# Kernel tuning notes

Measured on AMD Instinct MI355X. Metric: run time of the kernel, lower is better.

## Reference

```python
import jax, jax.numpy as jnp
import numpy as np

K = 4  # hard-coded in get_graph_feature


def knn_idx(x, k):
    # x: [B, C, N] -> idx [B, N, k] of nearest neighbors (largest negative sq dist)
    sq = jnp.sum(x * x, axis=1)                      # [B, N]
    inner = jnp.einsum('bcn,bcm->bnm', x, x)          # [B, N, N]
    pd = 2.0 * inner - sq[:, :, None] - sq[:, None, :]  # -||xi-xj||^2
    return jax.lax.top_k(pd, k)[1]                    # [B, N, k]


def get_graph_feature(x, k=K):
    # x: [B, C, N] -> [B, 2C, N, k]
    B = x.shape[0]
    idx = knn_idx(x, k)                               # [B, N, k]
    xt = jnp.transpose(x, (0, 2, 1))                  # [B, N, C]
    nbr = xt[jnp.arange(B)[:, None, None], idx]       # [B, N, k, C]
    ctr = jnp.broadcast_to(xt[:, :, None, :], nbr.shape)
    feat = jnp.concatenate([nbr, ctr], axis=-1)       # [B, N, k, 2C]
    return jnp.transpose(feat, (0, 3, 1, 2))          # [B, 2C, N, k]


def edge_block(x, W):
    # graph feature -> 1x1 conv -> relu -> max over k
    f = get_graph_feature(x)                          # [B, 2C, N, k]
    h = jax.nn.relu(jnp.einsum('oc,bcnk->bonk', W, f))
    return jnp.max(h, axis=-1)                        # [B, O, N]


def setup_inputs() -> dict:
    key = jax.random.key(0)
    ks = jax.random.split(key, 6)
    B, N, emb = 8, 2048, 512
    xavier = lambda k, o, c: jax.random.normal(k, (o, c), jnp.float32) * np.sqrt(2.0 / (o + c))
    return {
        'x': jax.random.normal(ks[0], (B, 3, N), jnp.float32),
        'W1': xavier(ks[1], 64, 6),
        'W2': xavier(ks[2], 64, 128),
        'W3': xavier(ks[3], 128, 128),
        'W4': xavier(ks[4], 256, 256),
        'W5': xavier(ks[5], emb, 512),
    }


def reference(x, W1, W2, W3, W4, W5):
    x1 = edge_block(x, W1)    # [B, 64, N]
    x2 = edge_block(x1, W2)   # [B, 64, N]
    x3 = edge_block(x2, W3)   # [B, 128, N]
    x4 = edge_block(x3, W4)   # [B, 256, N]
    feats = jnp.concatenate([x1, x2, x3, x4], axis=1)  # [B, 512, N]
    # if_relu_atlast=False path: final 1x1 conv, no activation
    return jnp.einsum('oc,bcn->bon', W5, feats)        # [B, emb, N]
```

## Files before the change

### kernel.cpp

```cpp
#include <hip/hip_runtime.h>
#include <hip/hip_bf16.h>

#define B_ 8
#define N_ 2048
#define SEG 8
#define TMM 64
#define TNN 128

typedef __bf16 bf16x8 __attribute__((ext_vector_type(8)));
typedef float  f32x4  __attribute__((ext_vector_type(4)));
typedef unsigned short u16;

__device__ __forceinline__ u16 f2bf(float f) {
    __hip_bfloat16 h = __float2bfloat16(f);
    return *reinterpret_cast<u16*>(&h);
}
__device__ __forceinline__ float bf2f(u16 u) {
    unsigned v = ((unsigned)u) << 16;
    return *reinterpret_cast<float*>(&v);
}

__global__ void k_transpose_x(const float* __restrict__ x, float* __restrict__ xt) {
    int i = blockIdx.x * 256 + threadIdx.x;
    if (i >= B_ * N_) return;
    int b = i >> 11, n = i & (N_ - 1);
    const float* src = x + (size_t)b * 3 * N_ + n;
    float* dst = xt + (size_t)i * 3;
    dst[0] = src[0];
    dst[1] = src[N_];
    dst[2] = src[2 * N_];
}

__global__ void k_sqnorm(const float* __restrict__ act, float* __restrict__ sq, int C) {
    int i = blockIdx.x * 256 + threadIdx.x;
    if (i >= B_ * N_) return;
    const float* r = act + (size_t)i * C;
    float s = 0.f;
    for (int c = 0; c < C; ++c) s += r[c] * r[c];
    sq[i] = s;
}

template<int C, int CP>
__global__ void k_split3(const float* __restrict__ act, u16* __restrict__ xh,
                         u16* __restrict__ xm, u16* __restrict__ xl) {
    int i = blockIdx.x * 256 + threadIdx.x;
    if (i >= B_ * N_ * CP / 8) return;
    int rn = i / (CP / 8), c8 = (i % (CP / 8)) * 8;
    u16 h[8], m[8], l[8];
    #pragma unroll
    for (int j = 0; j < 8; ++j) {
        int c = c8 + j;
        float x = (c < C) ? act[(size_t)rn * C + c] : 0.f;
        u16 hh = f2bf(x);
        float r1 = x - bf2f(hh);
        u16 mm = f2bf(r1);
        float r2 = r1 - bf2f(mm);
        h[j] = hh; m[j] = mm; l[j] = f2bf(r2);
    }
    *(uint4*)&xh[(size_t)i * 8] = *(uint4*)h;
    *(uint4*)&xm[(size_t)i * 8] = *(uint4*)m;
    *(uint4*)&xl[(size_t)i * 8] = *(uint4*)l;
}

__global__ void k_pack_w(const float* __restrict__ W, float* __restrict__ Wt,
                         int O, int C, int ncols, int wrow, int orow0) {
    int i = blockIdx.x * 256 + threadIdx.x;
    if (i >= C * ncols) return;
    int k = i / ncols, o2 = i % ncols;
    int o   = ((o2 < O) ? o2 : o2 - O) + orow0;
    int col = (o2 < O) ? k : (C + k);
    Wt[i] = W[(size_t)o * wrow + col];
}

__device__ __forceinline__ void ins4(float& v0, float& v1, float& v2, float& v3,
                                     int& i0, int& i1, int& i2, int& i3,
                                     float p, int m) {
    bool g3 = p > v3, g2 = p > v2, g1 = p > v1, g0 = p > v0;
    v3 = g2 ? v2 : (g3 ? p : v3); i3 = g2 ? i2 : (g3 ? m : i3);
    v2 = g1 ? v1 : (g2 ? p : v2); i2 = g1 ? i1 : (g2 ? m : i2);
    v1 = g0 ? v0 : (g1 ? p : v1); i1 = g0 ? i0 : (g1 ? m : i1);
    v0 = g0 ? p  : v0;            i0 = g0 ? m  : i0;
}

template<int CP>
__global__ __launch_bounds__(256) void k_knn_mfma(
    const u16* __restrict__ xh, const u16* __restrict__ xmd, const u16* __restrict__ xl,
    const float* __restrict__ sqg, float* __restrict__ pval, int* __restrict__ pidx)
{
    __shared__ __align__(16) u16 sm[3 * TNN * 40 + 3 * TMM * 40];
    __shared__ float sqm_l[TMM];
    u16* Anh = sm;
    u16* Anm = sm + TNN * 40;
    u16* Anl = sm + 2 * TNN * 40;
    u16* Amh = sm + 3 * TNN * 40;
    u16* Amm = Amh + TMM * 40;
    u16* Aml = Amh + 2 * TMM * 40;

    const int bid = blockIdx.x;
    const int seg = bid & (SEG - 1);
    const int nb  = (bid >> 3) & 15;
    const int b   = bid >> 7;
    const int n0  = nb * TNN;
    const int t    = threadIdx.x;
    const int w    = t >> 6, lane = t & 63;
    const int wm = w >> 1, wn = w & 1;
    const int l15 = lane & 15, l4 = lane >> 4;
    const size_t rowbase = (size_t)b * N_;

    float tv[4][4];
    int   ti[4][4];
    #pragma unroll
    for (int ni = 0; ni < 4; ++ni)
        #pragma unroll
        for (int q = 0; q < 4; ++q) { tv[ni][q] = -3.4e38f; ti[ni][q] = 0; }

    const int mstart = seg * (N_ / SEG);
    for (int m0 = mstart; m0 < mstart + N_ / SEG; m0 += TMM) {
        f32x4 acc[2][4];
        #pragma unroll
        for (int mi = 0; mi < 2; ++mi)
            #pragma unroll
            for (int ni = 0; ni < 4; ++ni) acc[mi][ni] = (f32x4){0.f, 0.f, 0.f, 0.f};

        for (int k0 = 0; k0 < CP; k0 += 32) {
            __syncthreads();
            for (int e = t; e < TNN * 4; e += 256) {
                int row = e >> 2, q = e & 3;
                size_t g = (rowbase + n0 + row) * CP + k0 + q * 8;
                int d = row * 40 + q * 8;
                *(uint4*)&Anh[d] = *(const uint4*)&xh[g];
                *(uint4*)&Anm[d] = *(const uint4*)&xmd[g];
                *(uint4*)&Anl[d] = *(const uint4*)&xl[g];
            }
            {
                int row = t >> 2, q = t & 3;
                size_t g = (rowbase + m0 + row) * CP + k0 + q * 8;
                int d = row * 40 + q * 8;
                *(uint4*)&Amh[d] = *(const uint4*)&xh[g];
                *(uint4*)&Amm[d] = *(const uint4*)&xmd[g];
                *(uint4*)&Aml[d] = *(const uint4*)&xl[g];
            }
            if (k0 == 0 && t < TMM) sqm_l[t] = sqg[rowbase + m0 + t];
            __syncthreads();

            bf16x8 amh[2], amm[2], aml[2], bnh[4], bnm[4], bnl[4];
            #pragma unroll
            for (int mi = 0; mi < 2; ++mi) {
                int off = (wm * 32 + mi * 16 + l15) * 40 + l4 * 8;
                amh[mi] = *(const bf16x8*)&Amh[off];
                amm[mi] = *(const bf16x8*)&Amm[off];
                aml[mi] = *(const bf16x8*)&Aml[off];
            }
            #pragma unroll
            for (int ni = 0; ni < 4; ++ni) {
                int off = (wn * 64 + ni * 16 + l15) * 40 + l4 * 8;
                bnh[ni] = *(const bf16x8*)&Anh[off];
                bnm[ni] = *(const bf16x8*)&Anm[off];
                bnl[ni] = *(const bf16x8*)&Anl[off];
            }
            #pragma unroll
            for (int mi = 0; mi < 2; ++mi)
                #pragma unroll
                for (int ni = 0; ni < 4; ++ni) {
                    f32x4 a = acc[mi][ni];
                    a = __builtin_amdgcn_mfma_f32_16x16x32_bf16(amh[mi], bnh[ni], a, 0, 0, 0);
                    a = __builtin_amdgcn_mfma_f32_16x16x32_bf16(amh[mi], bnm[ni], a, 0, 0, 0);
                    a = __builtin_amdgcn_mfma_f32_16x16x32_bf16(amm[mi], bnh[ni], a, 0, 0, 0);
                    a = __builtin_amdgcn_mfma_f32_16x16x32_bf16(amm[mi], bnm[ni], a, 0, 0, 0);
                    a = __builtin_amdgcn_mfma_f32_16x16x32_bf16(amh[mi], bnl[ni], a, 0, 0, 0);
                    a = __builtin_amdgcn_mfma_f32_16x16x32_bf16(aml[mi], bnh[ni], a, 0, 0, 0);
                    acc[mi][ni] = a;
                }
        }
        #pragma unroll
        for (int ni = 0; ni < 4; ++ni)
            #pragma unroll
            for (int mi = 0; mi < 2; ++mi)
                #pragma unroll
                for (int r = 0; r < 4; ++r) {
                    int mloc = wm * 32 + mi * 16 + l4 * 4 + r;
                    float sc = 2.f * acc[mi][ni][r] - sqm_l[mloc];
                    ins4(tv[ni][0], tv[ni][1], tv[ni][2], tv[ni][3],
                         ti[ni][0], ti[ni][1], ti[ni][2], ti[ni][3], sc, m0 + mloc);
                }
    }

    __syncthreads();
    float* sv = (float*)sm;
    int*   si = (int*)sm + 1024;
    #pragma unroll
    for (int ni = 0; ni < 4; ++ni) {
        float v0 = tv[ni][0], v1 = tv[ni][1], v2 = tv[ni][2], v3 = tv[ni][3];
        int   i0 = ti[ni][0], i1 = ti[ni][1], i2 = ti[ni][2], i3 = ti[ni][3];
        #pragma unroll
        for (int st = 16; st < 64; st <<= 1) {
            float w0 = __shfl_xor(v0, st), w1 = __shfl_xor(v1, st);
            float w2 = __shfl_xor(v2, st), w3 = __shfl_xor(v3, st);
            int   j0 = __shfl_xor(i0, st), j1 = __shfl_xor(i1, st);
            int   j2 = __shfl_xor(i2, st), j3 = __shfl_xor(i3, st);
            ins4(v0, v1, v2, v3, i0, i1, i2, i3, w0, j0);
            ins4(v0, v1, v2, v3, i0, i1, i2, i3, w1, j1);
            ins4(v0, v1, v2, v3, i0, i1, i2, i3, w2, j2);
            ins4(v0, v1, v2, v3, i0, i1, i2, i3, w3, j3);
        }
        if (l4 == 0) {
            int col = wn * 64 + ni * 16 + l15;
            int base = (wm * 128 + col) * 4;
            sv[base + 0] = v0; sv[base + 1] = v1; sv[base + 2] = v2; sv[base + 3] = v3;
            si[base + 0] = i0; si[base + 1] = i1; si[base + 2] = i2; si[base + 3] = i3;
        }
    }
    __syncthreads();
    if (t < 128) {
        int b0 = t * 4, b1 = (128 + t) * 4;
        float v0 = sv[b0], v1 = sv[b0 + 1], v2 = sv[b0 + 2], v3 = sv[b0 + 3];
        int   i0 = si[b0], i1 = si[b0 + 1], i2 = si[b0 + 2], i3 = si[b0 + 3];
        #pragma unroll
        for (int q = 0; q < 4; ++q)
            ins4(v0, v1, v2, v3, i0, i1, i2, i3, sv[b1 + q], si[b1 + q]);
        size_t pb = (rowbase + n0 + t) * (SEG * 4) + seg * 4;
        pval[pb + 0] = v0; pval[pb + 1] = v1; pval[pb + 2] = v2; pval[pb + 3] = v3;
        pidx[pb + 0] = i0; pidx[pb + 1] = i1; pidx[pb + 2] = i2; pidx[pb + 3] = i3;
    }
}

__global__ void k_knn_merge(const float* __restrict__ pval, const int* __restrict__ pidx,
                            int* __restrict__ idxo) {
    int rn = blockIdx.x * 256 + threadIdx.x;
    if (rn >= B_ * N_) return;
    const float* pv = pval + (size_t)rn * (SEG * 4);
    const int*   pi = pidx + (size_t)rn * (SEG * 4);
    float v0 = pv[0], v1 = pv[1], v2 = pv[2], v3 = pv[3];
    int   i0 = pi[0], i1 = pi[1], i2 = pi[2], i3 = pi[3];
    for (int s = 1; s < SEG; ++s)
        #pragma unroll
        for (int q = 0; q < 4; ++q)
            ins4(v0, v1, v2, v3, i0, i1, i2, i3, pv[s * 4 + q], pi[s * 4 + q]);
    int* op = idxo + (size_t)rn * 4;
    op[0] = i0; op[1] = i1; op[2] = i2; op[3] = i3;
}

__global__ __launch_bounds__(256) void k_gemm(
    const float* __restrict__ A, int lda,
    const float* __restrict__ Bt, int ldb,
    float* __restrict__ D, int ldd, int K)
{
    __shared__ float At[32 * 68];
    __shared__ float Bs[32 * 68];
    const int r0 = blockIdx.x * 64;
    const int c0 = blockIdx.y * 64;
    const int t  = threadIdx.x;
    const int tr = t >> 4, tc = t & 15;
    float acc[4][4];
    #pragma unroll
    for (int j = 0; j < 4; ++j)
        #pragma unroll
        for (int i = 0; i < 4; ++i) acc[j][i] = 0.f;

    for (int k0 = 0; k0 < K; k0 += 32) {
        for (int e = t; e < 64 * 32; e += 256) {
            int r = e >> 5, kk = e & 31;
            int kg = k0 + kk;
            float v = (kg < K) ? A[(size_t)(r0 + r) * lda + kg] : 0.f;
            At[kk * 68 + r] = v;
        }
        for (int e = t; e < 32 * 16; e += 256) {
            int kk = e >> 4, c4 = (e & 15) << 2;
            int kg = k0 + kk;
            float4 v = {0.f, 0.f, 0.f, 0.f};
            if (kg < K) v = *(const float4*)&Bt[(size_t)kg * ldb + c0 + c4];
            *(float4*)&Bs[kk * 68 + c4] = v;
        }
        __syncthreads();
        for (int kk = 0; kk < 32; ++kk) {
            float4 av = *(float4*)&At[kk * 68 + tr * 4];
            float4 bv = *(float4*)&Bs[kk * 68 + tc * 4];
            const float* ap = (const float*)&av;
            const float* bp = (const float*)&bv;
            #pragma unroll
            for (int j = 0; j < 4; ++j)
                #pragma unroll
                for (int i = 0; i < 4; ++i) acc[j][i] += ap[j] * bp[i];
        }
        __syncthreads();
    }

    #pragma unroll
    for (int j = 0; j < 4; ++j) {
        size_t r = r0 + tr * 4 + j;
        float4 v; v.x = acc[j][0]; v.y = acc[j][1]; v.z = acc[j][2]; v.w = acc[j][3];
        *(float4*)&D[r * ldd + c0 + tc * 4] = v;
    }
}

__global__ void k_gather_max(const float* __restrict__ dot, const int* __restrict__ idxg,
                             float* __restrict__ acto, int O, int ostride, int ocol0) {
    int i = blockIdx.x * 256 + threadIdx.x;
    if (i >= B_ * N_ * O) return;
    int o  = i % O;
    int rn = i / O;
    int b  = rn >> 11;
    const int* ip = idxg + (size_t)rn * 4;
    int twoO = O * 2;
    size_t bbase = (size_t)b * N_ * twoO;
    float ctr = dot[(size_t)rn * twoO + O + o];
    float m0 = dot[bbase + (size_t)ip[0] * twoO + o];
    float m1 = dot[bbase + (size_t)ip[1] * twoO + o];
    float m2 = dot[bbase + (size_t)ip[2] * twoO + o];
    float m3 = dot[bbase + (size_t)ip[3] * twoO + o];
    float mx = fmaxf(fmaxf(m0, m1), fmaxf(m2, m3));
    acto[(size_t)rn * ostride + ocol0 + o] = fmaxf(mx + ctr, 0.f);
}

__global__ void k_feat_bf16(const float* __restrict__ x1, const float* __restrict__ x2,
                            const float* __restrict__ x3, const float* __restrict__ x4,
                            u16* __restrict__ fb) {
    int i = blockIdx.x * 256 + threadIdx.x;
    if (i >= B_ * N_ * 512 / 8) return;
    int rn = i >> 6, c8 = (i & 63) << 3;
    const float* src;
    if      (c8 < 64)  src = x1 + (size_t)rn * 64  + c8;
    else if (c8 < 128) src = x2 + (size_t)rn * 64  + (c8 - 64);
    else if (c8 < 256) src = x3 + (size_t)rn * 128 + (c8 - 128);
    else               src = x4 + (size_t)rn * 256 + (c8 - 256);
    float4 va = *(const float4*)src;
    float4 vb = *(const float4*)(src + 4);
    uint4 u;
    u.x = ((unsigned)f2bf(va.y) << 16) | f2bf(va.x);
    u.y = ((unsigned)f2bf(va.w) << 16) | f2bf(va.z);
    u.z = ((unsigned)f2bf(vb.y) << 16) | f2bf(vb.x);
    u.w = ((unsigned)f2bf(vb.w) << 16) | f2bf(vb.z);
    *(uint4*)&fb[(size_t)i * 8] = u;
}

__global__ void k_w5_bf16(const float* __restrict__ W5, u16* __restrict__ wb) {
    int i = blockIdx.x * 256 + threadIdx.x;
    if (i >= 512 * 512 / 8) return;
    const float* src = W5 + (size_t)i * 8;
    float4 va = *(const float4*)src;
    float4 vb = *(const float4*)(src + 4);
    uint4 u;
    u.x = ((unsigned)f2bf(va.y) << 16) | f2bf(va.x);
    u.y = ((unsigned)f2bf(va.w) << 16) | f2bf(va.z);
    u.z = ((unsigned)f2bf(vb.y) << 16) | f2bf(vb.x);
    u.w = ((unsigned)f2bf(vb.w) << 16) | f2bf(vb.z);
    *(uint4*)&wb[(size_t)i * 8] = u;
}

__global__ __launch_bounds__(256) void k_mfma_final(
    const u16* __restrict__ Ab, const u16* __restrict__ Bb, float* __restrict__ out)
{
    __shared__ u16 As[128 * 40];
    __shared__ u16 Bs[128 * 40];
    const int bn0 = blockIdx.x * 128;
    const int o0  = blockIdx.y * 128;
    const int t    = threadIdx.x;
    const int w    = t >> 6;
    const int lane = t & 63;
    const int wm = w >> 1, wn = w & 1;
    const int l15 = lane & 15, l4 = lane >> 4;

    f32x4 acc[4][4];
    #pragma unroll
    for (int mi = 0; mi < 4; ++mi)
        #pragma unroll
        for (int ni = 0; ni < 4; ++ni) acc[mi][ni] = (f32x4){0.f, 0.f, 0.f, 0.f};

    for (int k0 = 0; k0 < 512; k0 += 32) {
        __syncthreads();
        for (int e = t; e < 128 * 4; e += 256) {
            int row = e >> 2, q = e & 3;
            *(float4*)&As[row * 40 + q * 8] =
                *(const float4*)&Ab[(size_t)(o0 + row) * 512 + k0 + q * 8];
            *(float4*)&Bs[row * 40 + q * 8] =
                *(const float4*)&Bb[(size_t)(bn0 + row) * 512 + k0 + q * 8];
        }
        __syncthreads();
        bf16x8 af[4], bf[4];
        #pragma unroll
        for (int mi = 0; mi < 4; ++mi)
            af[mi] = *(const bf16x8*)&As[(wm * 64 + mi * 16 + l15) * 40 + l4 * 8];
        #pragma unroll
        for (int ni = 0; ni < 4; ++ni)
            bf[ni] = *(const bf16x8*)&Bs[(wn * 64 + ni * 16 + l15) * 40 + l4 * 8];
        #pragma unroll
        for (int mi = 0; mi < 4; ++mi)
            #pragma unroll
            for (int ni = 0; ni < 4; ++ni)
                acc[mi][ni] = __builtin_amdgcn_mfma_f32_16x16x32_bf16(
                    af[mi], bf[ni], acc[mi][ni], 0, 0, 0);
    }

    const int bidx = bn0 >> 11;
    const int nloc = bn0 & (N_ - 1);
    #pragma unroll
    for (int mi = 0; mi < 4; ++mi)
        #pragma unroll
        for (int ni = 0; ni < 4; ++ni) {
            int o = o0 + wm * 64 + mi * 16 + l4 * 4;
            int n = nloc + wn * 64 + ni * 16 + l15;
            #pragma unroll
            for (int r = 0; r < 4; ++r)
                out[((size_t)bidx * 512 + o + r) * N_ + n] = acc[mi][ni][r];
        }
}

extern "C" void kernel_launch(void* const* d_in, const int* in_sizes, int n_in,
                              void* d_out, int out_size, void* d_ws, size_t ws_size,
                              hipStream_t stream) {
    const float* x  = (const float*)d_in[0];
    const float* W1 = (const float*)d_in[1];
    const float* W2 = (const float*)d_in[2];
    const float* W3 = (const float*)d_in[3];
    const float* W4 = (const float*)d_in[4];
    const float* W5 = (const float*)d_in[5];

    float* ws  = (float*)d_ws;
    float* x1  = ws;
    float* x2  = x1 + 1048576;
    float* x3  = x2 + 1048576;
    float* x4  = x3 + 2097152;
    float* dot = x4 + 4194304;
    float* xt0 = dot + 4194304;
    float* sq  = xt0 + 49152;
    int*   idx = (int*)(sq + 16384);
    float* wt  = sq + 16384 + 65536;
    u16*   xh   = (u16*)dot;
    u16*   xmd  = (u16*)(dot + 1048576);
    u16*   xl   = (u16*)(dot + 2097152);
    float* pval = dot + 3145728;
    int*   pidx = (int*)(dot + 3670016);
    u16*   featb = (u16*)dot;
    u16*   w5b   = (u16*)xt0;

    k_transpose_x<<<64, 256, 0, stream>>>(x, xt0);
    const int knn_grid = B_ * 16 * SEG;

    {
        const float* actin = xt0; int C = 3, O = 64, ncols = 2 * O;
        k_sqnorm<<<64, 256, 0, stream>>>(actin, sq, C);
        k_split3<3, 32><<<(B_ * N_ * 32 / 8 + 255) / 256, 256, 0, stream>>>(actin, xh, xmd, xl);
        k_knn_mfma<32><<<knn_grid, 256, 0, stream>>>(xh, xmd, xl, sq, pval, pidx);
        k_knn_merge<<<64, 256, 0, stream>>>(pval, pidx, idx);
        k_pack_w<<<(C * ncols + 255) / 256, 256, 0, stream>>>(W1, wt, O, C, ncols, 2 * C, 0);
        dim3 g((B_ * N_) / 64, ncols / 64);
        k_gemm<<<g, 256, 0, stream>>>(actin, C, wt, ncols, dot, ncols, C);
        k_gather_max<<<(B_ * N_ * O + 255) / 256, 256, 0, stream>>>(dot, idx, x1, O, O, 0);
    }
    {
        const float* actin = x1; int C = 64, O = 64, ncols = 2 * O;
        k_sqnorm<<<64, 256, 0, stream>>>(actin, sq, C);
        k_split3<64, 64><<<(B_ * N_ * 64 / 8 + 255) / 256, 256, 0, stream>>>(actin, xh, xmd, xl);
        k_knn_mfma<64><<<knn_grid, 256, 0, stream>>>(xh, xmd, xl, sq, pval, pidx);
        k_knn_merge<<<64, 256, 0, stream>>>(pval, pidx, idx);
        k_pack_w<<<(C * ncols + 255) / 256, 256, 0, stream>>>(W2, wt, O, C, ncols, 2 * C, 0);
        dim3 g((B_ * N_) / 64, ncols / 64);
        k_gemm<<<g, 256, 0, stream>>>(actin, C, wt, ncols, dot, ncols, C);
        k_gather_max<<<(B_ * N_ * O + 255) / 256, 256, 0, stream>>>(dot, idx, x2, O, O, 0);
    }
    {
        const float* actin = x2; int C = 64, O = 128, ncols = 2 * O;
        k_sqnorm<<<64, 256, 0, stream>>>(actin, sq, C);
        k_split3<64, 64><<<(B_ * N_ * 64 / 8 + 255) / 256, 256, 0, stream>>>(actin, xh, xmd, xl);
        k_knn_mfma<64><<<knn_grid, 256, 0, stream>>>(xh, xmd, xl, sq, pval, pidx);
        k_knn_merge<<<64, 256, 0, stream>>>(pval, pidx, idx);
        k_pack_w<<<(C * ncols + 255) / 256, 256, 0, stream>>>(W3, wt, O, C, ncols, 2 * C, 0);
        dim3 g((B_ * N_) / 64, ncols / 64);
        k_gemm<<<g, 256, 0, stream>>>(actin, C, wt, ncols, dot, ncols, C);
        k_gather_max<<<(B_ * N_ * O + 255) / 256, 256, 0, stream>>>(dot, idx, x3, O, O, 0);
    }
    {
        const float* actin = x3; int C = 128;
        k_sqnorm<<<64, 256, 0, stream>>>(actin, sq, C);
        k_split3<128, 128><<<(B_ * N_ * 128 / 8 + 255) / 256, 256, 0, stream>>>(actin, xh, xmd, xl);
        k_knn_mfma<128><<<knn_grid, 256, 0, stream>>>(xh, xmd, xl, sq, pval, pidx);
        k_knn_merge<<<64, 256, 0, stream>>>(pval, pidx, idx);
        for (int oh = 0; oh < 2; ++oh) {
            int Oh = 128, ncols = 2 * Oh, o0 = oh * 128;
            k_pack_w<<<(C * ncols + 255) / 256, 256, 0, stream>>>(W4, wt, Oh, C, ncols, 2 * C, o0);
            dim3 g((B_ * N_) / 64, ncols / 64);
            k_gemm<<<g, 256, 0, stream>>>(actin, C, wt, ncols, dot, ncols, C);
            k_gather_max<<<(B_ * N_ * Oh + 255) / 256, 256, 0, stream>>>(dot, idx, x4, Oh, 256, o0);
        }
    }

    k_feat_bf16<<<(B_ * N_ * 512 / 8 + 255) / 256, 256, 0, stream>>>(x1, x2, x3, x4, featb);
    k_w5_bf16<<<(512 * 512 / 8 + 255) / 256, 256, 0, stream>>>(W5, w5b);
    dim3 gm(B_ * N_ / 128, 512 / 128);
    k_mfma_final<<<gm, 256, 0, stream>>>(w5b, featb, (float*)d_out);
}
```

Measured before the change: 536.8 us.

## Replace FP32 SIMT conv GEMM with 3-way bf16-split MFMA GEMM

Replaces the scalar FP32 tiled GEMM for each edge-conv with an MFMA kernel. It reuses the hi/mid/lo bf16 split of the activations already produced for kNN and adds a matching three-way split of the packed weights, keeping six cross products to approximate FP32 accuracy. The dot buffer now lives in the output tensor, which frees workspace so layer 4 runs as one 512-column GEMM instead of two halves. The risks are small accuracy differences from the truncated split products and uncoalesced scalar stores in the epilogue.

Result: faster. 484.3 us (-9.8%).

```diff
diff --git a/kernel.cpp b/kernel.cpp
--- a/kernel.cpp
+++ b/kernel.cpp
@@ -62,14 +62,20 @@
     *(uint4*)&xl[(size_t)i * 8] = *(uint4*)l;
 }
 
-__global__ void k_pack_w(const float* __restrict__ W, float* __restrict__ Wt,
-                         int O, int C, int ncols, int wrow, int orow0) {
-    int i = blockIdx.x * 256 + threadIdx.x;
-    if (i >= C * ncols) return;
-    int k = i / ncols, o2 = i % ncols;
+__global__ void k_pack_wsplit3(const float* __restrict__ W, u16* __restrict__ wh,
+                               u16* __restrict__ wm, u16* __restrict__ wl,
+                               int O, int C, int CP, int ncols, int wrow, int orow0) {
+    int i = blockIdx.x * 256 + threadIdx.x;
+    if (i >= ncols * CP) return;
+    int o2 = i / CP, c = i % CP;
     int o   = ((o2 < O) ? o2 : o2 - O) + orow0;
-    int col = (o2 < O) ? k : (C + k);
-    Wt[i] = W[(size_t)o * wrow + col];
+    int col = (o2 < O) ? c : (C + c);
+    float v = (c < C) ? W[(size_t)o * wrow + col] : 0.f;
+    u16 hh = f2bf(v);
+    float r1 = v - bf2f(hh);
+    u16 mm = f2bf(r1);
+    float r2 = r1 - bf2f(mm);
+    wh[i] = hh; wm[i] = mm; wl[i] = f2bf(r2);
 }
 
 __device__ __forceinline__ void ins4(float& v0, float& v1, float& v2, float& v3,
@@ -240,57 +246,88 @@
     op[0] = i0; op[1] = i1; op[2] = i2; op[3] = i3;
 }
 
-__global__ __launch_bounds__(256) void k_gemm(
-    const float* __restrict__ A, int lda,
-    const float* __restrict__ Bt, int ldb,
-    float* __restrict__ D, int ldd, int K)
+template<int CP>
+__global__ __launch_bounds__(256) void k_conv_mfma(
+    const u16* __restrict__ xh, const u16* __restrict__ xmd, const u16* __restrict__ xl,
+    const u16* __restrict__ wh, const u16* __restrict__ wmm, const u16* __restrict__ wl,
+    float* __restrict__ D, int ncols)
 {
-    __shared__ float At[32 * 68];
-    __shared__ float Bs[32 * 68];
-    const int r0 = blockIdx.x * 64;
-    const int c0 = blockIdx.y * 64;
-    const int t  = threadIdx.x;
-    const int tr = t >> 4, tc = t & 15;
-    float acc[4][4];
-    #pragma unroll
-    for (int j = 0; j < 4; ++j)
-        #pragma unroll
-        for (int i = 0; i < 4; ++i) acc[j][i] = 0.f;
-
-    for (int k0 = 0; k0 < K; k0 += 32) {
-        for (int e = t; e < 64 * 32; e += 256) {
-            int r = e >> 5, kk = e & 31;
-            int kg = k0 + kk;
-            float v = (kg < K) ? A[(size_t)(r0 + r) * lda + kg] : 0.f;
-            At[kk * 68 + r] = v;
-        }
-        for (int e = t; e < 32 * 16; e += 256) {
-            int kk = e >> 4, c4 = (e & 15) << 2;
-            int kg = k0 + kk;
-            float4 v = {0.f, 0.f, 0.f, 0.f};
-            if (kg < K) v = *(const float4*)&Bt[(size_t)kg * ldb + c0 + c4];
-            *(float4*)&Bs[kk * 68 + c4] = v;
-        }
+    __shared__ __align__(16) u16 sm[6 * 128 * 40];
+    u16* Ah = sm;
+    u16* Am = sm + 128 * 40;
+    u16* Al = sm + 2 * 128 * 40;
+    u16* Bh = sm + 3 * 128 * 40;
+    u16* Bm = sm + 4 * 128 * 40;
+    u16* Bl = sm + 5 * 128 * 40;
+
+    const int bn0 = blockIdx.x * 128;
+    const int o0  = blockIdx.y * 128;
+    const int t    = threadIdx.x;
+    const int w    = t >> 6, lane = t & 63;
+    const int wm = w >> 1, wn = w & 1;
+    const int l15 = lane & 15, l4 = lane >> 4;
+
+    f32x4 acc[4][4];
+    #pragma unroll
+    for (int mi = 0; mi < 4; ++mi)
+        #pragma unroll
+        for (int ni = 0; ni < 4; ++ni) acc[mi][ni] = (f32x4){0.f, 0.f, 0.f, 0.f};
+
+    for (int k0 = 0; k0 < CP; k0 += 32) {
         __syncthreads();
-        for (int kk = 0; kk < 32; ++kk) {
-            float4 av = *(float4*)&At[kk * 68 + tr * 4];
-            float4 bv = *(float4*)&Bs[kk * 68 + tc * 4];
-            const float* ap = (const float*)&av;
-            const float* bp = (const float*)&bv;
-            #pragma unroll
-            for (int j = 0; j < 4; ++j)
-                #pragma unroll
-                for (int i = 0; i < 4; ++i) acc[j][i] += ap[j] * bp[i];
+        for (int e = t; e < 128 * 4; e += 256) {
+            int row = e >> 2, q = e & 3;
+            int d = row * 40 + q * 8;
+            size_t ga = (size_t)(bn0 + row) * CP + k0 + q * 8;
+            size_t gb = (size_t)(o0 + row) * CP + k0 + q * 8;
+            *(uint4*)&Ah[d] = *(const uint4*)&xh[ga];
+            *(uint4*)&Am[d] = *(const uint4*)&xmd[ga];
+            *(uint4*)&Al[d] = *(const uint4*)&xl[ga];
+            *(uint4*)&Bh[d] = *(const uint4*)&wh[gb];
+            *(uint4*)&Bm[d] = *(const uint4*)&wmm[gb];
+            *(uint4*)&Bl[d] = *(const uint4*)&wl[gb];
         }
         __syncthreads();
-    }
-
-    #pragma unroll
-    for (int j = 0; j < 4; ++j) {
-        size_t r = r0 + tr * 4 + j;
-        float4 v; v.x = acc[j][0]; v.y = acc[j][1]; v.z = acc[j][2]; v.w = acc[j][3];
-        *(float4*)&D[r * ldd + c0 + tc * 4] = v;
-    }
+        bf16x8 ah[4], am[4], al[4], bh[4], bm[4], bl[4];
+        #pragma unroll
+        for (int mi = 0; mi < 4; ++mi) {
+            int off = (wm * 64 + mi * 16 + l15) * 40 + l4 * 8;
+            ah[mi] = *(const bf16x8*)&Ah[off];
+            am[mi] = *(const bf16x8*)&Am[off];
+            al[mi] = *(const bf16x8*)&Al[off];
+        }
+        #pragma unroll
+        for (int ni = 0; ni < 4; ++ni) {
+            int off = (wn * 64 + ni * 16 + l15) * 40 + l4 * 8;
+            bh[ni] = *(const bf16x8*)&Bh[off];
+            bm[ni] = *(const bf16x8*)&Bm[off];
+            bl[ni] = *(const bf16x8*)&Bl[off];
+        }
+        #pragma unroll
+        for (int mi = 0; mi < 4; ++mi)
+            #pragma unroll
+            for (int ni = 0; ni < 4; ++ni) {
+                f32x4 a = acc[mi][ni];
+                a = __builtin_amdgcn_mfma_f32_16x16x32_bf16(ah[mi], bh[ni], a, 0, 0, 0);
+                a = __builtin_amdgcn_mfma_f32_16x16x32_bf16(ah[mi], bm[ni], a, 0, 0, 0);
+                a = __builtin_amdgcn_mfma_f32_16x16x32_bf16(am[mi], bh[ni], a, 0, 0, 0);
+                a = __builtin_amdgcn_mfma_f32_16x16x32_bf16(am[mi], bm[ni], a, 0, 0, 0);
+                a = __builtin_amdgcn_mfma_f32_16x16x32_bf16(ah[mi], bl[ni], a, 0, 0, 0);
+                a = __builtin_amdgcn_mfma_f32_16x16x32_bf16(al[mi], bh[ni], a, 0, 0, 0);
+                acc[mi][ni] = a;
+            }
+    }
+
+    #pragma unroll
+    for (int mi = 0; mi < 4; ++mi)
+        #pragma unroll
+        for (int ni = 0; ni < 4; ++ni) {
+            int bnl_ = wm * 64 + mi * 16 + l4 * 4;
+            int o2  = o0 + wn * 64 + ni * 16 + l15;
+            #pragma unroll
+            for (int r = 0; r < 4; ++r)
+                D[(size_t)(bn0 + bnl_ + r) * ncols + o2] = acc[mi][ni][r];
+        }
 }
 
 __global__ void k_gather_max(const float* __restrict__ dot, const int* __restrict__ idxg,
@@ -420,68 +457,73 @@
     float* x2  = x1 + 1048576;
     float* x3  = x2 + 1048576;
     float* x4  = x3 + 2097152;
-    float* dot = x4 + 4194304;
-    float* xt0 = dot + 4194304;
+    float* dreg = x4 + 4194304;
+    float* xt0 = dreg + 4194304;
     float* sq  = xt0 + 49152;
     int*   idx = (int*)(sq + 16384);
     float* wt  = sq + 16384 + 65536;
-    u16*   xh   = (u16*)dot;
-    u16*   xmd  = (u16*)(dot + 1048576);
-    u16*   xl   = (u16*)(dot + 2097152);
-    float* pval = dot + 3145728;
-    int*   pidx = (int*)(dot + 3670016);
-    u16*   featb = (u16*)dot;
+    u16*   xh   = (u16*)dreg;
+    u16*   xmd  = (u16*)(dreg + 1048576);
+    u16*   xl   = (u16*)(dreg + 2097152);
+    float* pval = dreg + 3145728;
+    int*   pidx = (int*)(dreg + 3670016);
+    u16*   featb = (u16*)dreg;
     u16*   w5b   = (u16*)xt0;
+    u16*   woh = (u16*)wt;
+    u16*   wom = woh + 65536;
+    u16*   wol = wom + 65536;
+    float* dot = (float*)d_out;
 
     k_transpose_x<<<64, 256, 0, stream>>>(x, xt0);
     const int knn_grid = B_ * 16 * SEG;
 
     {
-        const float* actin = xt0; int C = 3, O = 64, ncols = 2 * O;
+        const float* actin = xt0; int C = 3, O = 64, ncols = 2 * O, CP = 32;
         k_sqnorm<<<64, 256, 0, stream>>>(actin, sq, C);
         k_split3<3, 32><<<(B_ * N_ * 32 / 8 + 255) / 256, 256, 0, stream>>>(actin, xh, xmd, xl);
         k_knn_mfma<32><<<knn_grid, 256, 0, stream>>>(xh, xmd, xl, sq, pval, pidx);
         k_knn_merge<<<64, 256, 0, stream>>>(pval, pidx, idx);
-        k_pack_w<<<(C * ncols + 255) / 256, 256, 0, stream>>>(W1, wt, O, C, ncols, 2 * C, 0);
-        dim3 g((B_ * N_) / 64, ncols / 64);
-        k_gemm<<<g, 256, 0, stream>>>(actin, C, wt, ncols, dot, ncols, C);
+        k_pack_wsplit3<<<(ncols * CP + 255) / 256, 256, 0, stream>>>(W1, woh, wom, wol,
+                                                                     O, C, CP, ncols, 2 * C, 0);
+        dim3 g((B_ * N_) / 128, ncols / 128);
+        k_conv_mfma<32><<<g, 256, 0, stream>>>(xh, xmd, xl, woh, wom, wol, dot, ncols);
         k_gather_max<<<(B_ * N_ * O + 255) / 256, 256, 0, stream>>>(dot, idx, x1, O, O, 0);
     }
     {
-        const float* actin = x1; int C = 64, O = 64, ncols = 2 * O;
+        const float* actin = x1; int C = 64, O = 64, ncols = 2 * O, CP = 64;
         k_sqnorm<<<64, 256, 0, stream>>>(actin, sq, C);
         k_split3<64, 64><<<(B_ * N_ * 64 / 8 + 255) / 256, 256, 0, stream>>>(actin, xh, xmd, xl);
         k_knn_mfma<64><<<knn_grid, 256, 0, stream>>>(xh, xmd, xl, sq, pval, pidx);
         k_knn_merge<<<64, 256, 0, stream>>>(pval, pidx, idx);
-        k_pack_w<<<(C * ncols + 255) / 256, 256, 0, stream>>>(W2, wt, O, C, ncols, 2 * C, 0);
-        dim3 g((B_ * N_) / 64, ncols / 64);
-        k_gemm<<<g, 256, 0, stream>>>(actin, C, wt, ncols, dot, ncols, C);
+        k_pack_wsplit3<<<(ncols * CP + 255) / 256, 256, 0, stream>>>(W2, woh, wom, wol,
+                                                                     O, C, CP, ncols, 2 * C, 0);
+        dim3 g((B_ * N_) / 128, ncols / 128);
+        k_conv_mfma<64><<<g, 256, 0, stream>>>(xh, xmd, xl, woh, wom, wol, dot, ncols);
         k_gather_max<<<(B_ * N_ * O + 255) / 256, 256, 0, stream>>>(dot, idx, x2, O, O, 0);
     }
     {
-        const float* actin = x2; int C = 64, O = 128, ncols = 2 * O;
+        const float* actin = x2; int C = 64, O = 128, ncols = 2 * O, CP = 64;
         k_sqnorm<<<64, 256, 0, stream>>>(actin, sq, C);
         k_split3<64, 64><<<(B_ * N_ * 64 / 8 + 255) / 256, 256, 0, stream>>>(actin, xh, xmd, xl);
         k_knn_mfma<64><<<knn_grid, 256, 0, stream>>>(xh, xmd, xl, sq, pval, pidx);
         k_knn_merge<<<64, 256, 0, stream>>>(pval, pidx, idx);
-        k_pack_w<<<(C * ncols + 255) / 256, 256, 0, stream>>>(W3, wt, O, C, ncols, 2 * C, 0);
-        dim3 g((B_ * N_) / 64, ncols / 64);
-        k_gemm<<<g, 256, 0, stream>>>(actin, C, wt, ncols, dot, ncols, C);
+        k_pack_wsplit3<<<(ncols * CP + 255) / 256, 256, 0, stream>>>(W3, woh, wom, wol,
+                                                                     O, C, CP, ncols, 2 * C, 0);
+        dim3 g((B_ * N_) / 128, ncols / 128);
+        k_conv_mfma<64><<<g, 256, 0, stream>>>(xh, xmd, xl, woh, wom, wol, dot, ncols);
         k_gather_max<<<(B_ * N_ * O + 255) / 256, 256, 0, stream>>>(dot, idx, x3, O, O, 0);
     }
     {
-        const float* actin = x3; int C = 128;
+        const float* actin = x3; int C = 128, O = 256, ncols = 2 * O, CP = 128;
         k_sqnorm<<<64, 256, 0, stream>>>(actin, sq, C);
         k_split3<128, 128><<<(B_ * N_ * 128 / 8 + 255) / 256, 256, 0, stream>>>(actin, xh, xmd, xl);
         k_knn_mfma<128><<<knn_grid, 256, 0, stream>>>(xh, xmd, xl, sq, pval, pidx);
         k_knn_merge<<<64, 256, 0, stream>>>(pval, pidx, idx);
-        for (int oh = 0; oh < 2; ++oh) {
-            int Oh = 128, ncols = 2 * Oh, o0 = oh * 128;
-            k_pack_w<<<(C * ncols + 255) / 256, 256, 0, stream>>>(W4, wt, Oh, C, ncols, 2 * C, o0);
-            dim3 g((B_ * N_) / 64, ncols / 64);
-            k_gemm<<<g, 256, 0, stream>>>(actin, C, wt, ncols, dot, ncols, C);
-            k_gather_max<<<(B_ * N_ * Oh + 255) / 256, 256, 0, stream>>>(dot, idx, x4, Oh, 256, o0);
-        }
+        k_pack_wsplit3<<<(ncols * CP + 255) / 256, 256, 0, stream>>>(W4, woh, wom, wol,
+                                                                     O, C, CP, ncols, 2 * C, 0);
+        dim3 g((B_ * N_) / 128, ncols / 128);
+        k_conv_mfma<128><<<g, 256, 0, stream>>>(xh, xmd, xl, woh, wom, wol, dot, ncols);
+        k_gather_max<<<(B_ * N_ * O + 255) / 256, 256, 0, stream>>>(dot, idx, x4, O, O, 0);
     }
 
     k_feat_bf16<<<(B_ * N_ * 512 / 8 + 255) / 256, 256, 0, stream>>>(x1, x2, x3, x4, featb);
```
